# Kernel optimization log

Measured on AMD Instinct MI355X. Metric: run time of the kernel, lower is better.

## Reference

```python
import jax, jax.numpy as jnp
import numpy as np

R = 16      # grid resolution per axis (G = R**3 voxels)
K = 8       # num KNN neighbors per voxel
H = 64      # num_hidden
NB = 2      # num conv blocks
EPS = 1e-5


def _conv3d(x, w, b):
    # x: [B,C,D,H,W], w: [O,I,3,3,3]
    y = jax.lax.conv_general_dilated(
        x, w, window_strides=(1, 1, 1), padding='SAME',
        dimension_numbers=('NCDHW', 'OIDHW', 'NCDHW'))
    return y + b[None, :, None, None, None]


def _bn(x):
    # training-mode BatchNorm3d statistics (no affine), per channel
    m = x.mean(axis=(0, 2, 3, 4), keepdims=True)
    v = x.var(axis=(0, 2, 3, 4), keepdims=True)
    return (x - m) * jax.lax.rsqrt(v + EPS)


def _forward(pos, x, pe_w1, pe_b1, pe_w2, pe_b2, f_w, f_b, up_w, up_b,
             conv_w, conv_b, on_g, on_b, ro_w, ro_b):
    B, N, _ = pos.shape
    # ---- Gridifier: coordinate grid over domain [-1, 1]^3 ----
    g1 = jnp.linspace(-1.0, 1.0, R, dtype=pos.dtype)
    grid = jnp.stack(jnp.meshgrid(g1, g1, g1, indexing='ij'), axis=-1).reshape(-1, 3)  # [G,3]
    # ---- brute-force KNN: points -> grid voxels (per graph) ----
    gn = jnp.sum(grid * grid, axis=-1)          # [G]
    pn = jnp.sum(pos * pos, axis=-1)            # [B,N]
    d = gn[None, :, None] + pn[:, None, :] - 2.0 * jnp.einsum('gc,bnc->bgn', grid, pos)  # [B,G,N]
    idx = jax.lax.top_k(jax.lax.stop_gradient(-d), K)[1]  # [B,G,K] nearest point indices
    b_ix = jnp.arange(B)[:, None, None]
    p_nb = pos[b_ix, idx]                       # [B,G,K,3] neighbor positions
    f_nb = x[b_ix, idx]                         # [B,G,K,Cin] neighbor features
    # ---- BipartiteConv: position-conditioned messages, mean aggregation ----
    rel = p_nb - grid[None, :, None, :]         # relative positions [B,G,K,3]
    pe = jax.nn.gelu(rel @ pe_w1 + pe_b1) @ pe_w2 + pe_b2   # position embed [B,G,K,H]
    msg = pe * (f_nb @ f_w + f_b)               # multiplicative conditioning [B,G,K,H]
    agg = msg.mean(axis=2)                      # [B,G,H]
    h = jax.nn.gelu(agg @ up_w + up_b)          # update net [B,G,H]
    # reshape(B,R,R,R,H).permute(0,4,3,2,1) -> NCDHW
    vol = h.reshape(B, R, R, R, H).transpose(0, 4, 3, 2, 1)  # [B,H,R,R,R]
    # ---- ConvNet3D: residual blocks, maxpool after block 0 ----
    for i in range(NB):
        h1 = jax.nn.relu(_bn(_conv3d(vol, conv_w[i, 0], conv_b[i, 0])))
        h2 = _bn(_conv3d(h1, conv_w[i, 1], conv_b[i, 1]))
        vol = jax.nn.relu(vol + h2)
        if i == 0:
            vol = jax.lax.reduce_window(vol, -jnp.inf, jax.lax.max,
                                        (1, 1, 2, 2, 2), (1, 1, 2, 2, 2), 'VALID')
    out = _bn(vol) * on_g[None, :, None, None, None] + on_b[None, :, None, None, None]
    # ---- mean readout pool + linear head ----
    pooled = out.mean(axis=(2, 3, 4))           # [B,H]
    return pooled @ ro_w + ro_b                 # [B,out_channels]


def setup_inputs() -> dict:
    key = jax.random.key(0)
    ks = jax.random.split(key, 10)
    B, N, Cin, OUT = 4, 4096, 3, 16
    s = 0.05
    return {
        'pos': jax.random.uniform(ks[0], (B, N, 3), jnp.float32, -1.0, 1.0),
        'x': jax.random.normal(ks[1], (B, N, Cin), jnp.float32),
        'pe_w1': jax.random.normal(ks[2], (3, H), jnp.float32) * 0.3,
        'pe_b1': jnp.zeros((H,), jnp.float32),
        'pe_w2': jax.random.normal(ks[3], (H, H), jnp.float32) * s,
        'pe_b2': jnp.zeros((H,), jnp.float32),
        'f_w': jax.random.normal(ks[4], (Cin, H), jnp.float32) * 0.3,
        'f_b': jnp.zeros((H,), jnp.float32),
        'up_w': jax.random.normal(ks[5], (H, H), jnp.float32) * s,
        'up_b': jnp.zeros((H,), jnp.float32),
        'conv_w': jax.random.normal(ks[6], (NB, 2, H, H, 3, 3, 3), jnp.float32) * s,
        'conv_b': jnp.zeros((NB, 2, H), jnp.float32),
        'on_g': jnp.ones((H,), jnp.float32),
        'on_b': jnp.zeros((H,), jnp.float32),
        'ro_w': jax.random.normal(ks[7], (H, OUT), jnp.float32) * s,
        'ro_b': jnp.zeros((OUT,), jnp.float32),
    }


def reference(pos, x, pe_w1, pe_b1, pe_w2, pe_b2, f_w, f_b, up_w, up_b,
              conv_w, conv_b, on_g, on_b, ro_w, ro_b):
    return _forward(pos, x, pe_w1, pe_b1, pe_w2, pe_b2, f_w, f_b, up_w, up_b,
                    conv_w, conv_b, on_g, on_b, ro_w, ro_b)
```

## Files before the change

kernel.cpp:

```cpp
#include <hip/hip_runtime.h>

#define ULL unsigned long long
typedef unsigned short ush;
typedef __attribute__((ext_vector_type(8))) short s8v;
typedef __attribute__((ext_vector_type(4))) float f4v;

#define BB 4
#define NP 4096
#define HH 64
#define EPSF 1e-5f

#define WH_OFF      0u
#define WL_OFF      221184u
#define WT_PER_CONV 110592u
#define IDX_OFF     442368u
#define VOL0_OFF    573440u
#define V0H_OFF     2066432u
#define V0L_OFF     2812928u
#define T1_OFF      3559424u
#define VOL1_OFF    4608000u
#define V1H_OFF     4864000u
#define V1L_OFF     4992000u
#define T3_OFF      5120000u
#define STATS_OFF   5251072u
#define CELLS_OFF   5251968u
#define SPOS_OFF    5268368u
#define MW_OFF      5333904u

#define ZN_V0   373248u
#define ZN_V1   64000u
#define ZN_ST   224u
#define ZN_ALL  (ZN_V0 + ZN_V1 + ZN_ST)

__device__ __forceinline__ ush f2bf(float f) {
  unsigned u = __float_as_uint(f);
  return (ush)((u + 0x7FFFu + ((u >> 16) & 1u)) >> 16);
}
__device__ __forceinline__ float bf2f(ush h) { return __uint_as_float(((unsigned)h) << 16); }

__device__ __forceinline__ float gelu_tanh(float v) {
  float inner = 0.7978845608028654f * (v + 0.044715f * v * v * v);
  return 0.5f * v * (1.0f + tanhf(inner));
}

__device__ __forceinline__ float lin16(int i) {
  return -1.0f + (float)i * (2.0f / 15.0f);
}

__global__ __launch_bounds__(256) void k_prep(const float* __restrict__ cw,
                                              const float* __restrict__ pw2,
                                              const float* __restrict__ upw,
                                              ush* __restrict__ wh,
                                              ush* __restrict__ wl,
                                              ush* __restrict__ mw,
                                              float* __restrict__ ws) {
  unsigned i = blockIdx.x * 256u + threadIdx.x;
  float4 z = make_float4(0.f, 0.f, 0.f, 0.f);
  if (i < ZN_V0) ((float4*)(ws + V0H_OFF))[i] = z;
  else if (i < ZN_V0 + ZN_V1) ((float4*)(ws + V1H_OFF))[i - ZN_V0] = z;
  else if (i < ZN_ALL) ((float4*)(ws + STATS_OFF))[i - ZN_V0 - ZN_V1] = z;
  if (i < 442368u) {
    unsigned conv = i / WT_PER_CONV;
    unsigned r = i - conv * WT_PER_CONV;
    unsigned off = r >> 12;
    unsigned q = r & 4095u;
    unsigned co = q >> 6, ci = q & 63u;
    float w = cw[(conv * 4096u + co * 64u + ci) * 27u + off];
    ush hi = f2bf(w);
    wh[i] = hi;
    wl[i] = f2bf(w - bf2f(hi));
  } else if (i < 450560u) {
    unsigned t = i - 442368u;
    unsigned mat = t >> 12, r = t & 4095u;
    unsigned co = r >> 6, ci = r & 63u;
    const float* src = mat ? upw : pw2;
    float w = src[ci * 64u + co];
    ush hi = f2bf(w);
    mw[mat * 8192u + co * 64u + ci] = hi;
    mw[mat * 8192u + 4096u + co * 64u + ci] = f2bf(w - bf2f(hi));
  }
}

__global__ __launch_bounds__(256) void k_bin(const float* __restrict__ pos,
                                             int* __restrict__ cellStart,
                                             float4* __restrict__ sortedPos) {
  __shared__ int cnt[4096];
  __shared__ int wsum[4];
  int tid = threadIdx.x;
  int b = blockIdx.x;
  const float* pb = pos + b * NP * 3;
  for (int i = tid; i < 4096; i += 256) cnt[i] = 0;
  __syncthreads();
#pragma unroll
  for (int t = 0; t < 16; ++t) {
    int p = t * 256 + tid;
    float px = pb[3 * p], py = pb[3 * p + 1], pz = pb[3 * p + 2];
    int c0 = (int)floorf((px + 1.0f) * 7.5f + 0.5f);
    int c1 = (int)floorf((py + 1.0f) * 7.5f + 0.5f);
    int c2 = (int)floorf((pz + 1.0f) * 7.5f + 0.5f);
    c0 = min(max(c0, 0), 15); c1 = min(max(c1, 0), 15); c2 = min(max(c2, 0), 15);
    atomicAdd(&cnt[(c0 * 16 + c1) * 16 + c2], 1);
  }
  __syncthreads();
  int base = tid * 16;
  int loc[16];
  int run = 0;
#pragma unroll
  for (int j = 0; j < 16; ++j) { loc[j] = run; run += cnt[base + j]; }
  int lane = tid & 63, wv = tid >> 6;
  int inc = run;
  for (int d = 1; d < 64; d <<= 1) {
    int o = __shfl_up(inc, d, 64);
    if (lane >= d) inc += o;
  }
  if (lane == 63) wsum[wv] = inc;
  __syncthreads();
  int woff = 0;
  for (int w = 0; w < wv; ++w) woff += wsum[w];
  int excl = woff + inc - run;
  __syncthreads();
  int stv[16];
#pragma unroll
  for (int j = 0; j < 16; ++j) {
    stv[j] = excl + loc[j];
    cellStart[b * 4097 + base + j] = stv[j];
  }
#pragma unroll
  for (int j = 0; j < 16; ++j) cnt[base + j] = stv[j];
  if (tid == 0) cellStart[b * 4097 + 4096] = NP;
  __syncthreads();
#pragma unroll
  for (int t = 0; t < 16; ++t) {
    int p = t * 256 + tid;
    float px = pb[3 * p], py = pb[3 * p + 1], pz = pb[3 * p + 2];
    int c0 = (int)floorf((px + 1.0f) * 7.5f + 0.5f);
    int c1 = (int)floorf((py + 1.0f) * 7.5f + 0.5f);
    int c2 = (int)floorf((pz + 1.0f) * 7.5f + 0.5f);
    c0 = min(max(c0, 0), 15); c1 = min(max(c1, 0), 15); c2 = min(max(c2, 0), 15);
    int slot = atomicAdd(&cnt[(c0 * 16 + c1) * 16 + c2], 1);
    sortedPos[b * 4096 + slot] = make_float4(px, py, pz, __int_as_float(p));
  }
}

__global__ __launch_bounds__(64) void k_knn2(const int* __restrict__ cellStart,
                                             const float4* __restrict__ sortedPos,
                                             int* __restrict__ idxo) {
  __shared__ int cs[4097];
  int tid = threadIdx.x;
  int vox = blockIdx.x * 64 + tid;
  int b = vox >> 12;
  int g = vox & 4095;
  for (int i = tid; i < 4097; i += 64) cs[i] = cellStart[b * 4097 + i];
  __syncthreads();
  int ii = g >> 8, jj = (g >> 4) & 15, kkc = g & 15;
  float gx = lin16(ii), gy = lin16(jj), gz = lin16(kkc);
  float gn = gx * gx + gy * gy + gz * gz;
  const float4* sp = sortedPos + b * 4096;
  ULL kk[8];
#pragma unroll
  for (int q = 0; q < 8; ++q) kk[q] = ~0ULL;
  for (int s = 0; s < 16; ++s) {
    int alo = max(ii - s, 0), ahi = min(ii + s, 15);
    int blo = max(jj - s, 0), bhi = min(jj + s, 15);
    int clo = max(kkc - s, 0), chi = min(kkc + s, 15);
    for (int a = alo; a <= ahi; ++a)
      for (int b2 = blo; b2 <= bhi; ++b2) {
        bool edge = (a == ii - s) || (a == ii + s) || (b2 == jj - s) || (b2 == jj + s);
        int cbase = (a * 16 + b2) * 16;
        int r0lo, r0hi, r1lo, r1hi;
        if (edge) { r0lo = clo; r0hi = chi; r1lo = 1; r1hi = 0; }
        else {
          r0lo = kkc - s; r0hi = kkc - s;
          if (kkc - s < 0) { r0lo = 1; r0hi = 0; }
          r1lo = kkc + s; r1hi = kkc + s;
          if (kkc + s > 15) { r1lo = 1; r1hi = 0; }
        }
#pragma unroll
        for (int rr = 0; rr < 2; ++rr) {
          int rlo = rr ? r1lo : r0lo, rhi = rr ? r1hi : r0hi;
          if (rlo > rhi) continue;
          int st = cs[cbase + rlo], en = cs[cbase + rhi + 1];
          for (int t = st; t < en; ++t) {
            float4 c = sp[t];
            float px = c.x, py = c.y, pz = c.z;
            float pn = px * px + py * py + pz * pz;
            float dt = gx * px + gy * py + gz * pz;
            float d = (gn + pn) - 2.0f * dt;
            unsigned u = __float_as_uint(d);
            u ^= (unsigned)((int)u >> 31) | 0x80000000u;
            ULL key = ((ULL)u << 32) | (unsigned)__float_as_uint(c.w);
            if (key < kk[7]) {
              kk[7] = key;
#pragma unroll
              for (int q2 = 7; q2 >= 1; --q2) {
                ULL x0 = kk[q2 - 1], x1 = kk[q2];
                bool sw = x1 < x0;
                kk[q2 - 1] = sw ? x1 : x0;
                kk[q2] = sw ? x0 : x1;
              }
            }
          }
        }
      }
    float bnd = ((float)s + 0.5f) * (2.0f / 15.0f) - 1e-5f;
    float b2f = bnd * bnd;
    unsigned ub = __float_as_uint(b2f) | 0x80000000u;
    if (((ULL)ub << 32) > kk[7]) break;
  }
#pragma unroll
  for (int q = 0; q < 8; ++q)
    idxo[(((b << 12) | g) << 3) + q] = (int)(kk[q] & 0xFFFFFFFFULL);
}

__global__ __launch_bounds__(256) void k_mlp2(
    const float* __restrict__ pos, const float* __restrict__ xf,
    const float* __restrict__ w1, const float* __restrict__ b1,
    const float* __restrict__ b2v, const float* __restrict__ fw,
    const float* __restrict__ fb, const float* __restrict__ ub,
    const ush* __restrict__ w2tH, const ush* __restrict__ w2tL,
    const ush* __restrict__ uwtH, const ush* __restrict__ uwtL,
    const int* __restrict__ idx, float* __restrict__ vol0,
    ush* __restrict__ v0h, ush* __restrict__ v0l) {
  __shared__ __align__(16) ush lhH[128 * 72];
  __shared__ __align__(16) ush lhL[128 * 72];
  __shared__ __align__(16) float lfe[128 * 68];
  __shared__ __align__(16) ush agH[16 * 72];
  __shared__ __align__(16) ush agL[16 * 72];
  int tid = threadIdx.x, lane = tid & 63, wv = tid >> 6;
  int lm = lane & 15, quad = lane >> 4;
  int b = blockIdx.x >> 8;
  int g0 = (blockIdx.x & 255) << 4;
  s8v BH[8], BL[8], UH[2], UL[2];
#pragma unroll
  for (int n = 0; n < 4; ++n)
#pragma unroll
    for (int ks = 0; ks < 2; ++ks) {
      int o = ((n * 16 + lm) << 6) + ks * 32 + (quad << 3);
      BH[n * 2 + ks] = *(const s8v*)(w2tH + o);
      BL[n * 2 + ks] = *(const s8v*)(w2tL + o);
    }
#pragma unroll
  for (int ks = 0; ks < 2; ++ks) {
    int o = ((wv * 16 + lm) << 6) + ks * 32 + (quad << 3);
    UH[ks] = *(const s8v*)(uwtH + o);
    UL[ks] = *(const s8v*)(uwtL + o);
  }
  float w10 = w1[lane], w11 = w1[64 + lane], w12 = w1[128 + lane], b1c = b1[lane];
  float fw0 = fw[lane], fw1 = fw[64 + lane], fw2 = fw[128 + lane], fbc = fb[lane];
  float gx = lin16(g0 >> 8), gy = lin16((g0 >> 4) & 15);
  for (int i = 0; i < 32; ++i) {
    int pair = wv * 32 + i;
    int vi = pair >> 3, kk = pair & 7;
    int g = g0 + vi;
    float gz = lin16(vi);
    int p = idx[(((b << 12) | g) << 3) + kk];
    const float* pp = pos + (b * NP + p) * 3;
    float r0 = pp[0] - gx, r1 = pp[1] - gy, r2 = pp[2] - gz;
    float h1 = gelu_tanh(fmaf(r2, w12, fmaf(r1, w11, fmaf(r0, w10, b1c))));
    const float* xp = xf + (b * NP + p) * 3;
    float fe = fmaf(xp[2], fw2, fmaf(xp[1], fw1, fmaf(xp[0], fw0, fbc)));
    ush hi = f2bf(h1);
    lhH[pair * 72 + lane] = hi;
    lhL[pair * 72 + lane] = f2bf(h1 - bf2f(hi));
    lfe[pair * 68 + lane] = fe;
  }
  f4v acc[2][4];
#pragma unroll
  for (int m = 0; m < 2; ++m)
#pragma unroll
    for (int n = 0; n < 4; ++n) acc[m][n] = (f4v){0.f, 0.f, 0.f, 0.f};
#pragma unroll
  for (int m = 0; m < 2; ++m)
#pragma unroll
    for (int ks = 0; ks < 2; ++ks) {
      int ao = (wv * 32 + m * 16 + lm) * 72 + ks * 32 + quad * 8;
      s8v Ah = *(const s8v*)&lhH[ao];
      s8v Al = *(const s8v*)&lhL[ao];
#pragma unroll
      for (int n = 0; n < 4; ++n) {
        acc[m][n] = __builtin_amdgcn_mfma_f32_16x16x32_bf16(Ah, BH[n * 2 + ks], acc[m][n], 0, 0, 0);
        acc[m][n] = __builtin_amdgcn_mfma_f32_16x16x32_bf16(Ah, BL[n * 2 + ks], acc[m][n], 0, 0, 0);
        acc[m][n] = __builtin_amdgcn_mfma_f32_16x16x32_bf16(Al, BH[n * 2 + ks], acc[m][n], 0, 0, 0);
      }
    }
  float b2c[4];
#pragma unroll
  for (int n = 0; n < 4; ++n) b2c[n] = b2v[n * 16 + lm];
#pragma unroll
  for (int m = 0; m < 2; ++m) {
    int vox = wv * 4 + m * 2 + (quad >> 1);
#pragma unroll
    for (int n = 0; n < 4; ++n) {
      float s = 0.0f;
#pragma unroll
      for (int r = 0; r < 4; ++r) {
        int pair = wv * 32 + m * 16 + quad * 4 + r;
        s += (acc[m][n][r] + b2c[n]) * lfe[pair * 68 + n * 16 + lm];
      }
      s += __shfl_xor(s, 16, 64);
      s *= 0.125f;
      if ((quad & 1) == 0) {
        ush hi = f2bf(s);
        agH[vox * 72 + n * 16 + lm] = hi;
        agL[vox * 72 + n * 16 + lm] = f2bf(s - bf2f(hi));
      }
    }
  }
  __syncthreads();
  f4v a2 = (f4v){0.f, 0.f, 0.f, 0.f};
#pragma unroll
  for (int ks = 0; ks < 2; ++ks) {
    int ao = lm * 72 + ks * 32 + quad * 8;
    s8v Ah = *(const s8v*)&agH[ao];
    s8v Al = *(const s8v*)&agL[ao];
    a2 = __builtin_amdgcn_mfma_f32_16x16x32_bf16(Ah, UH[ks], a2, 0, 0, 0);
    a2 = __builtin_amdgcn_mfma_f32_16x16x32_bf16(Ah, UL[ks], a2, 0, 0, 0);
    a2 = __builtin_amdgcn_mfma_f32_16x16x32_bf16(Al, UH[ks], a2, 0, 0, 0);
  }
  float ubc = ub[wv * 16 + lm];
  int xc = g0 >> 8, yc = (g0 >> 4) & 15;
#pragma unroll
  for (int r = 0; r < 4; ++r) {
    int vox = quad * 4 + r;
    float h = gelu_tanh(a2[r] + ubc);
    int pidx = (((b * 18 + vox + 1) * 18 + yc + 1) * 18 + xc + 1) * 64 + wv * 16 + lm;
    vol0[pidx] = h;
    ush hi = f2bf(h);
    v0h[pidx] = hi;
    v0l[pidx] = f2bf(h - bf2f(hi));
  }
}

template <int Z>
__global__ __launch_bounds__(256) void k_convm(const ush* __restrict__ vh,
                                               const ush* __restrict__ vl,
                                               const ush* __restrict__ wh,
                                               const ush* __restrict__ wl,
                                               float* __restrict__ out,
                                               float* __restrict__ stats) {
  constexpr int P = Z + 2;
  constexpr int Py = (Z == 16) ? 6 : 10;
  constexpr int Px = (Z == 16) ? 18 : 10;
  constexpr int NV = 3 * Py * Px;
  constexpr int VS = 272;
  __shared__ unsigned char slab[NV * VS];
  __shared__ float ls[64], ls2[64];
  int tid = threadIdx.x;
  int lane = tid & 63, wv = tid >> 6;
  int vbase = blockIdx.x * 64;
  int b = (Z == 16) ? (vbase >> 12) : (vbase >> 9);
  int rem = vbase & (Z * Z * Z - 1);
  int z0 = rem / (Z * Z);
  int y0 = (Z == 16) ? ((rem & 255) >> 4) : 0;
  if (tid < 64) { ls[tid] = 0.0f; ls2[tid] = 0.0f; }
  {
    constexpr int NCH = NV * 8;
    for (int i = tid; i < NCH; i += 256) {
      int v = i >> 3, c = i & 7;
      int lz = v / (Py * Px);
      int r = v - lz * (Py * Px);
      int ly = r / Px, lx = r - ly * Px;
      int g = (((b * P + z0 + lz) * P + (y0 + ly)) * P + lx) * 64 + c * 8;
      *(uint4*)(slab + v * VS + c * 16)       = *(const uint4*)(vh + g);
      *(uint4*)(slab + v * VS + 128 + c * 16) = *(const uint4*)(vl + g);
    }
  }
  __syncthreads();
  int lm = lane & 15, quad = lane >> 4;
  int co = (wv << 4) | lm;
  f4v acc[4];
#pragma unroll
  for (int m = 0; m < 4; ++m) acc[m] = (f4v){0.f, 0.f, 0.f, 0.f};
  for (int off = 0; off < 27; ++off) {
    int dz = off / 9, r9 = off - dz * 9, dy = r9 / 3, dx = r9 - dy * 3;
    const ush* bph = wh + ((off * 64 + co) << 6) + (quad << 3);
    const ush* bpl = wl + ((off * 64 + co) << 6) + (quad << 3);
#pragma unroll
    for (int ks = 0; ks < 2; ++ks) {
      s8v bhf = *(const s8v*)(bph + ks * 32);
      s8v blf = *(const s8v*)(bpl + ks * 32);
#pragma unroll
      for (int m = 0; m < 4; ++m) {
        int lyp, lxp;
        if (Z == 16) { lyp = m + dy; lxp = lm + dx; }
        else         { lyp = 2 * m + (lm >> 3) + dy; lxp = (lm & 7) + dx; }
        int sv = (dz * Py + lyp) * Px + lxp;
        const unsigned char* ap = slab + sv * VS + (quad << 4) + (ks << 6);
        s8v ahf = *(const s8v*)(ap);
        s8v alf = *(const s8v*)(ap + 128);
        acc[m] = __builtin_amdgcn_mfma_f32_16x16x32_bf16(ahf, bhf, acc[m], 0, 0, 0);
        acc[m] = __builtin_amdgcn_mfma_f32_16x16x32_bf16(ahf, blf, acc[m], 0, 0, 0);
        acc[m] = __builtin_amdgcn_mfma_f32_16x16x32_bf16(alf, bhf, acc[m], 0, 0, 0);
      }
    }
  }
  float s = 0.0f, s2 = 0.0f;
#pragma unroll
  for (int m = 0; m < 4; ++m) {
    int vx = vbase + (m << 4) + (quad << 2);
#pragma unroll
    for (int r = 0; r < 4; ++r) {
      float v = acc[m][r];
      out[(vx + r) * 64 + co] = v;
      s += v;
      s2 = fmaf(v, v, s2);
    }
  }
  atomicAdd(&ls[co], s);
  atomicAdd(&ls2[co], s2);
  __syncthreads();
  if (tid < 64) {
    atomicAdd(&stats[tid * 2], ls[tid]);
    atomicAdd(&stats[tid * 2 + 1], ls2[tid]);
  }
}

template <int Z>
__global__ __launch_bounds__(256) void k_bnrelu(const float* __restrict__ t,
                                                const float* __restrict__ stats,
                                                ush* __restrict__ outh,
                                                ush* __restrict__ outl,
                                                float inv_cnt) {
  constexpr int P = Z + 2;
  unsigned i = blockIdx.x * 256u + threadIdx.x;
  int c = i & 63;
  int vox = i >> 6;
  int x = vox % Z;
  int q = vox / Z;
  int y = q % Z;
  q /= Z;
  int z = q % Z;
  int b = q / Z;
  float m = stats[c * 2] * inv_cnt;
  float var = stats[c * 2 + 1] * inv_cnt - m * m;
  float rs = 1.0f / sqrtf(var + EPSF);
  float v = (t[i] - m) * rs;
  v = v > 0.0f ? v : 0.0f;
  int pidx = (((b * P + z + 1) * P + y + 1) * P + x + 1) * 64 + c;
  ush hi = f2bf(v);
  outh[pidx] = hi;
  outl[pidx] = f2bf(v - bf2f(hi));
}

__global__ __launch_bounds__(256) void k_residpool(const float* __restrict__ vol0,
                                                   const float* __restrict__ t2,
                                                   const float* __restrict__ stats,
                                                   float* __restrict__ vol1,
                                                   ush* __restrict__ v1h,
                                                   ush* __restrict__ v1l) {
  unsigned i = blockIdx.x * 256u + threadIdx.x;
  int c = i & 63;
  int pv = i >> 6;
  int xp = pv & 7, yp = (pv >> 3) & 7, zp = (pv >> 6) & 7, b = pv >> 9;
  float m = stats[c * 2] * (1.0f / 16384.0f);
  float var = stats[c * 2 + 1] * (1.0f / 16384.0f) - m * m;
  float rs = 1.0f / sqrtf(var + EPSF);
  float best = 0.0f;
  for (int dz = 0; dz < 2; ++dz)
    for (int dy = 0; dy < 2; ++dy)
      for (int dx = 0; dx < 2; ++dx) {
        int z = 2 * zp + dz, y = 2 * yp + dy, x = 2 * xp + dx;
        float a = vol0[(((b * 18 + z + 1) * 18 + y + 1) * 18 + x + 1) * 64 + c];
        float t = t2[(b * 4096 + z * 256 + y * 16 + x) * 64 + c];
        float u = a + (t - m) * rs;
        u = u > 0.0f ? u : 0.0f;
        best = u > best ? u : best;
      }
  int pidx = (((b * 10 + zp + 1) * 10 + yp + 1) * 10 + xp + 1) * 64 + c;
  vol1[pidx] = best;
  ush hi = f2bf(best);
  v1h[pidx] = hi;
  v1l[pidx] = f2bf(best - bf2f(hi));
}

__global__ __launch_bounds__(256) void k_resid2(const float* __restrict__ vol1,
                                                const float* __restrict__ t4,
                                                const float* __restrict__ stats,
                                                float* __restrict__ sF,
                                                float* __restrict__ sB) {
  __shared__ float ls[64], ls2[64];
  if (threadIdx.x < 64) { ls[threadIdx.x] = 0.0f; ls2[threadIdx.x] = 0.0f; }
  __syncthreads();
  unsigned i = blockIdx.x * 256u + threadIdx.x;
  int c = i & 63;
  int pv = i >> 6;
  int x = pv & 7, y = (pv >> 3) & 7, z = (pv >> 6) & 7, b = pv >> 9;
  float m = stats[c * 2] * (1.0f / 2048.0f);
  float var = stats[c * 2 + 1] * (1.0f / 2048.0f) - m * m;
  float rs = 1.0f / sqrtf(var + EPSF);
  float a = vol1[(((b * 10 + z + 1) * 10 + y + 1) * 10 + x + 1) * 64 + c];
  float u = a + (t4[i] - m) * rs;
  u = u > 0.0f ? u : 0.0f;
  atomicAdd(&ls[c], u);
  atomicAdd(&ls2[c], u * u);
  __syncthreads();
  if (threadIdx.x < 64) {
    int cc = threadIdx.x;
    atomicAdd(&sF[cc * 2], ls[cc]);
    atomicAdd(&sF[cc * 2 + 1], ls2[cc]);
    atomicAdd(&sB[b * 64 + cc], ls[cc]);
  }
}

__global__ __launch_bounds__(64) void k_final(const float* __restrict__ sF,
                                              const float* __restrict__ sB,
                                              const float* __restrict__ ong,
                                              const float* __restrict__ onb,
                                              const float* __restrict__ row,
                                              const float* __restrict__ rob,
                                              float* __restrict__ outp) {
  __shared__ float pl[4][64];
  int c = threadIdx.x;
  float m = sF[c * 2] * (1.0f / 2048.0f);
  float var = sF[c * 2 + 1] * (1.0f / 2048.0f) - m * m;
  float rs = 1.0f / sqrtf(var + EPSF);
  float gg = ong[c], bb = onb[c];
  for (int b = 0; b < 4; ++b)
    pl[b][c] = (sB[b * 64 + c] * (1.0f / 512.0f) - m) * rs * gg + bb;
  __syncthreads();
  int b = threadIdx.x >> 4, o = threadIdx.x & 15;
  float s = rob[o];
  for (int j = 0; j < 64; ++j) s = fmaf(pl[b][j], row[j * 16 + o], s);
  outp[b * 16 + o] = s;
}

extern "C" void kernel_launch(void* const* d_in, const int* in_sizes, int n_in,
                              void* d_out, int out_size, void* d_ws, size_t ws_size,
                              hipStream_t stream) {
  (void)in_sizes; (void)n_in; (void)out_size; (void)ws_size;
  const float* pos = (const float*)d_in[0];
  const float* xf  = (const float*)d_in[1];
  const float* pw1 = (const float*)d_in[2];
  const float* pb1 = (const float*)d_in[3];
  const float* pw2 = (const float*)d_in[4];
  const float* pb2 = (const float*)d_in[5];
  const float* fw  = (const float*)d_in[6];
  const float* fb  = (const float*)d_in[7];
  const float* uw  = (const float*)d_in[8];
  const float* ubp = (const float*)d_in[9];
  const float* cw  = (const float*)d_in[10];
  const float* ong = (const float*)d_in[12];
  const float* onb = (const float*)d_in[13];
  const float* row = (const float*)d_in[14];
  const float* rob = (const float*)d_in[15];

  float* ws   = (float*)d_ws;
  ush*   wh   = (ush*)(ws + WH_OFF);
  ush*   wl   = (ush*)(ws + WL_OFF);
  int*   idx  = (int*)(ws + IDX_OFF);
  float* vol0 = ws + VOL0_OFF;
  ush*   v0h  = (ush*)(ws + V0H_OFF);
  ush*   v0l  = (ush*)(ws + V0L_OFF);
  float* t1   = ws + T1_OFF;
  float* vol1 = ws + VOL1_OFF;
  ush*   v1h  = (ush*)(ws + V1H_OFF);
  ush*   v1l  = (ush*)(ws + V1L_OFF);
  float* t3   = ws + T3_OFF;
  float* sA   = ws + STATS_OFF;
  float* sF   = sA + 512;
  float* sB   = sF + 128;
  int*   cellStart = (int*)(ws + CELLS_OFF);
  float4* sortedPos = (float4*)(ws + SPOS_OFF);
  ush*   mw   = (ush*)(ws + MW_OFF);

  k_prep<<<1760, 256, 0, stream>>>(cw, pw2, uw, wh, wl, mw, ws);
  k_bin<<<4, 256, 0, stream>>>(pos, cellStart, sortedPos);
  k_knn2<<<256, 64, 0, stream>>>(cellStart, sortedPos, idx);
  k_mlp2<<<1024, 256, 0, stream>>>(pos, xf, pw1, pb1, pb2, fw, fb, ubp,
                                   mw, mw + 4096, mw + 8192, mw + 12288,
                                   idx, vol0, v0h, v0l);
  k_convm<16><<<256, 256, 0, stream>>>(v0h, v0l, wh, wl, t1, sA);
  k_bnrelu<16><<<4096, 256, 0, stream>>>(t1, sA, v0h, v0l, 1.0f / 16384.0f);
  k_convm<16><<<256, 256, 0, stream>>>(v0h, v0l, wh + WT_PER_CONV, wl + WT_PER_CONV,
                                       t1, sA + 128);
  k_residpool<<<512, 256, 0, stream>>>(vol0, t1, sA + 128, vol1, v1h, v1l);
  k_convm<8><<<32, 256, 0, stream>>>(v1h, v1l, wh + 2 * WT_PER_CONV,
                                     wl + 2 * WT_PER_CONV, t3, sA + 256);
  k_bnrelu<8><<<512, 256, 0, stream>>>(t3, sA + 256, v1h, v1l, 1.0f / 2048.0f);
  k_convm<8><<<32, 256, 0, stream>>>(v1h, v1l, wh + 3 * WT_PER_CONV,
                                     wl + 3 * WT_PER_CONV, t3, sA + 384);
  k_resid2<<<512, 256, 0, stream>>>(vol1, t3, sA + 384, sF, sB);
  k_final<<<1, 64, 0, stream>>>(sF, sB, ong, onb, row, rob, (float*)d_out);
}
```

Baseline: 349.3 us.

## Split KNN search across 8 lanes per voxel with fixed 5x5x5 cell window

Replaces the one-thread-per-voxel expanding-shell KNN with eight threads per voxel. Each thread scans a strided subset of a fixed 5x5x5 neighbourhood of cells, and the eight partial top-8 lists are merged with wave shuffles. If the merged 8th distance exceeds the radius the window guarantees, all points are brute-force scanned. This raises parallelism and occupancy for the KNN stage (512 blocks of 256 threads instead of 256 blocks of 64), at the cost of reading cellStart from global memory and scanning more cells than the adaptive search. It also hoists the update-bias load in the MLP kernel.

```diff
diff --git a/kernel.cpp b/kernel.cpp
--- a/kernel.cpp
+++ b/kernel.cpp
@@ -142,74 +142,89 @@
   }
 }
 
-__global__ __launch_bounds__(64) void k_knn2(const int* __restrict__ cellStart,
-                                             const float4* __restrict__ sortedPos,
-                                             int* __restrict__ idxo) {
-  __shared__ int cs[4097];
+__device__ __forceinline__ void ins8(ULL* kk, ULL key) {
+  if (key < kk[7]) {
+    kk[7] = key;
+#pragma unroll
+    for (int q = 7; q >= 1; --q) {
+      ULL a = kk[q - 1], c = kk[q];
+      bool sw = c < a;
+      kk[q - 1] = sw ? c : a;
+      kk[q] = sw ? a : c;
+    }
+  }
+}
+__device__ __forceinline__ ULL merge8(ULL* kk, int sub) {
+  ULL win = 0;
+#pragma unroll
+  for (int r = 0; r < 8; ++r) {
+    ULL m = kk[0];
+#pragma unroll
+    for (int s = 1; s < 8; s <<= 1) {
+      ULL o = __shfl_xor(m, s, 64);
+      m = (o < m) ? o : m;
+    }
+    if (kk[0] == m) {
+#pragma unroll
+      for (int q = 0; q < 7; ++q) kk[q] = kk[q + 1];
+      kk[7] = ~0ULL;
+    }
+    if (sub == r) win = m;
+  }
+  return win;
+}
+
+__global__ __launch_bounds__(256) void k_knn3(const int* __restrict__ cellStart,
+                                              const float4* __restrict__ sortedPos,
+                                              int* __restrict__ idxo) {
   int tid = threadIdx.x;
-  int vox = blockIdx.x * 64 + tid;
+  int sub = tid & 7;
+  int vox = blockIdx.x * 32 + (tid >> 3);
   int b = vox >> 12;
   int g = vox & 4095;
-  for (int i = tid; i < 4097; i += 64) cs[i] = cellStart[b * 4097 + i];
-  __syncthreads();
   int ii = g >> 8, jj = (g >> 4) & 15, kkc = g & 15;
   float gx = lin16(ii), gy = lin16(jj), gz = lin16(kkc);
   float gn = gx * gx + gy * gy + gz * gz;
+  const int* cs = cellStart + b * 4097;
   const float4* sp = sortedPos + b * 4096;
   ULL kk[8];
 #pragma unroll
   for (int q = 0; q < 8; ++q) kk[q] = ~0ULL;
-  for (int s = 0; s < 16; ++s) {
-    int alo = max(ii - s, 0), ahi = min(ii + s, 15);
-    int blo = max(jj - s, 0), bhi = min(jj + s, 15);
-    int clo = max(kkc - s, 0), chi = min(kkc + s, 15);
-    for (int a = alo; a <= ahi; ++a)
-      for (int b2 = blo; b2 <= bhi; ++b2) {
-        bool edge = (a == ii - s) || (a == ii + s) || (b2 == jj - s) || (b2 == jj + s);
-        int cbase = (a * 16 + b2) * 16;
-        int r0lo, r0hi, r1lo, r1hi;
-        if (edge) { r0lo = clo; r0hi = chi; r1lo = 1; r1hi = 0; }
-        else {
-          r0lo = kkc - s; r0hi = kkc - s;
-          if (kkc - s < 0) { r0lo = 1; r0hi = 0; }
-          r1lo = kkc + s; r1hi = kkc + s;
-          if (kkc + s > 15) { r1lo = 1; r1hi = 0; }
-        }
-#pragma unroll
-        for (int rr = 0; rr < 2; ++rr) {
-          int rlo = rr ? r1lo : r0lo, rhi = rr ? r1hi : r0hi;
-          if (rlo > rhi) continue;
-          int st = cs[cbase + rlo], en = cs[cbase + rhi + 1];
-          for (int t = st; t < en; ++t) {
-            float4 c = sp[t];
-            float px = c.x, py = c.y, pz = c.z;
-            float pn = px * px + py * py + pz * pz;
-            float dt = gx * px + gy * py + gz * pz;
-            float d = (gn + pn) - 2.0f * dt;
-            unsigned u = __float_as_uint(d);
-            u ^= (unsigned)((int)u >> 31) | 0x80000000u;
-            ULL key = ((ULL)u << 32) | (unsigned)__float_as_uint(c.w);
-            if (key < kk[7]) {
-              kk[7] = key;
-#pragma unroll
-              for (int q2 = 7; q2 >= 1; --q2) {
-                ULL x0 = kk[q2 - 1], x1 = kk[q2];
-                bool sw = x1 < x0;
-                kk[q2 - 1] = sw ? x1 : x0;
-                kk[q2] = sw ? x0 : x1;
-              }
-            }
-          }
-        }
-      }
-    float bnd = ((float)s + 0.5f) * (2.0f / 15.0f) - 1e-5f;
-    float b2f = bnd * bnd;
-    unsigned ub = __float_as_uint(b2f) | 0x80000000u;
-    if (((ULL)ub << 32) > kk[7]) break;
-  }
-#pragma unroll
-  for (int q = 0; q < 8; ++q)
-    idxo[(((b << 12) | g) << 3) + q] = (int)(kk[q] & 0xFFFFFFFFULL);
+  for (int t = sub; t < 125; t += 8) {
+    int dz = t / 25, r25 = t - dz * 25;
+    int a = ii + dz - 2, c1 = jj + (r25 / 5) - 2, c2 = kkc + (r25 % 5) - 2;
+    if (((unsigned)a > 15u) | ((unsigned)c1 > 15u) | ((unsigned)c2 > 15u)) continue;
+    int cell = (a * 16 + c1) * 16 + c2;
+    int st = cs[cell], en = cs[cell + 1];
+    for (int p = st; p < en; ++p) {
+      float4 c = sp[p];
+      float pn = c.x * c.x + c.y * c.y + c.z * c.z;
+      float dt = gx * c.x + gy * c.y + gz * c.z;
+      float d = (gn + pn) - 2.0f * dt;
+      unsigned u = __float_as_uint(d);
+      u ^= (unsigned)((int)u >> 31) | 0x80000000u;
+      ins8(kk, ((ULL)u << 32) | (unsigned)__float_as_uint(c.w));
+    }
+  }
+  ULL win = merge8(kk, sub);
+  float bnd = 2.5f * (2.0f / 15.0f) - 1e-5f;
+  unsigned ub = __float_as_uint(bnd * bnd) | 0x80000000u;
+  ULL w7 = __shfl(win, 7, 8);
+  if (w7 >= ((ULL)ub << 32)) {
+#pragma unroll
+    for (int q = 0; q < 8; ++q) kk[q] = ~0ULL;
+    for (int p = sub; p < NP; p += 8) {
+      float4 c = sp[p];
+      float pn = c.x * c.x + c.y * c.y + c.z * c.z;
+      float dt = gx * c.x + gy * c.y + gz * c.z;
+      float d = (gn + pn) - 2.0f * dt;
+      unsigned u = __float_as_uint(d);
+      u ^= (unsigned)((int)u >> 31) | 0x80000000u;
+      ins8(kk, ((ULL)u << 32) | (unsigned)__float_as_uint(c.w));
+    }
+    win = merge8(kk, sub);
+  }
+  idxo[(((b << 12) | g) << 3) + sub] = (int)(win & 0xFFFFFFFFULL);
 }
 
 __global__ __launch_bounds__(256) void k_mlp2(
@@ -247,6 +262,7 @@
   }
   float w10 = w1[lane], w11 = w1[64 + lane], w12 = w1[128 + lane], b1c = b1[lane];
   float fw0 = fw[lane], fw1 = fw[64 + lane], fw2 = fw[128 + lane], fbc = fb[lane];
+  float ubc = ub[wv * 16 + lm];
   float gx = lin16(g0 >> 8), gy = lin16((g0 >> 4) & 15);
   for (int i = 0; i < 32; ++i) {
     int pair = wv * 32 + i;
@@ -317,7 +333,6 @@
     a2 = __builtin_amdgcn_mfma_f32_16x16x32_bf16(Ah, UL[ks], a2, 0, 0, 0);
     a2 = __builtin_amdgcn_mfma_f32_16x16x32_bf16(Al, UH[ks], a2, 0, 0, 0);
   }
-  float ubc = ub[wv * 16 + lm];
   int xc = g0 >> 8, yc = (g0 >> 4) & 15;
 #pragma unroll
   for (int r = 0; r < 4; ++r) {
@@ -565,7 +580,7 @@
 
   k_prep<<<1760, 256, 0, stream>>>(cw, pw2, uw, wh, wl, mw, ws);
   k_bin<<<4, 256, 0, stream>>>(pos, cellStart, sortedPos);
-  k_knn2<<<256, 64, 0, stream>>>(cellStart, sortedPos, idx);
+  k_knn3<<<512, 256, 0, stream>>>(cellStart, sortedPos, idx);
   k_mlp2<<<1024, 256, 0, stream>>>(pos, xf, pw1, pb1, pb2, fw, fb, ubp,
                                    mw, mw + 4096, mw + 8192, mw + 12288,
                                    idx, vol0, v0h, v0l);
```

Measured after the change: 504.9 us. 44.6% more time.
